# Performance work log

Measured on AMD Instinct MI355X. Metric: run time of the kernel, lower is better.

Reference implementation:

```python
import jax, jax.numpy as jnp
import numpy as np

NSAMPLE = 16
LEAKY = 0.1


def _leaky(x):
    return jnp.where(x >= 0, x, LEAKY * x)


def _sqdist(src, dst):
    # src [B,N,3], dst [B,M,3] -> [B,N,M]
    d = -2.0 * jnp.einsum('bnc,bmc->bnm', src, dst)
    d = d + jnp.sum(src * src, -1)[:, :, None]
    d = d + jnp.sum(dst * dst, -1)[:, None, :]
    return d


def _knn_idx(query, points, k):
    # query [B,N,3], points [B,M,3] -> [B,N,k] indices of k nearest points
    dist = _sqdist(query, points)
    _, idx = jax.lax.top_k(-dist, k)
    return idx


def _group(points, idx):
    # points [B,M,C], idx [B,N,K] -> [B,N,K,C]
    return jax.vmap(lambda p, i: p[i])(points, idx)


def _cross(xyz1, xyz2, p1, p2, pos_w, pos_b, mlp_params):
    # xyz1 [B,N1,3], xyz2 [B,N2,3], p1 [B,N1,C], p2 [B,N2,C]
    idx = _knn_idx(xyz1, xyz2, NSAMPLE)                       # [B,N1,K]
    neigh_xyz = _group(xyz2, idx)                             # [B,N1,K,3]
    direction = neigh_xyz - xyz1[:, :, None, :]               # [B,N1,K,3]
    g2 = _group(p2, idx)                                      # [B,N1,K,C]
    pos_feat = jnp.einsum('bnkc,oc->bnko', direction, pos_w) + pos_b
    new_pts = _leaky(g2 + p1[:, :, None, :] + pos_feat)       # [B,N1,K,C0]
    for w, b in mlp_params:
        new_pts = _leaky(jnp.einsum('bnkc,oc->bnko', new_pts, w) + b)
    return jnp.max(new_pts, axis=2)                           # [B,N1,Cl]


def setup_inputs() -> dict:
    key = jax.random.key(0)
    ks = jax.random.split(key, 14)
    B, N, D = 2, 8192, 64
    s = 0.1
    return {
        'pc1': jax.random.normal(ks[0], (B, N, 3), jnp.float32),
        'pc2': jax.random.normal(ks[1], (B, N, 3), jnp.float32),
        'feat1': jax.random.normal(ks[2], (B, N, D), jnp.float32),
        'feat2': jax.random.normal(ks[3], (B, N, D), jnp.float32),
        'pos_w': jax.random.normal(ks[4], (64, 3), jnp.float32) * s,
        'pos_b': jax.random.normal(ks[5], (64,), jnp.float32) * s,
        'mlp_w0': jax.random.normal(ks[6], (64, 64), jnp.float32) * s,
        'mlp_b0': jax.random.normal(ks[7], (64,), jnp.float32) * s,
        'mlp_w1': jax.random.normal(ks[8], (64, 64), jnp.float32) * s,
        'mlp_b1': jax.random.normal(ks[9], (64,), jnp.float32) * s,
        't1_w': jax.random.normal(ks[10], (128, 64), jnp.float32) * s,
        't1_b': jax.random.normal(ks[11], (128,), jnp.float32) * s,
        't2_w': jax.random.normal(ks[12], (128, 64), jnp.float32) * s,
        't2_b': jax.random.normal(ks[13], (128,), jnp.float32) * s,
    }


def reference(pc1, pc2, feat1, feat2, pos_w, pos_b, mlp_w0, mlp_b0,
              mlp_w1, mlp_b1, t1_w, t1_b, t2_w, t2_b):
    mlp = [(mlp_w0, mlp_b0), (mlp_w1, mlp_b1)]
    f1 = _cross(pc1, pc2, feat1, feat2, pos_w, pos_b, mlp)    # [B,N1,64]
    f1 = jnp.einsum('bnc,oc->bno', f1, t1_w) + t1_b           # [B,N1,128]
    f2 = _cross(pc2, pc1, feat2, feat1, pos_w, pos_b, mlp)
    f2 = jnp.einsum('bnc,oc->bno', f2, t2_w) + t2_b
    return f1, f2
```

## Files before the change

kernel.cpp:

```cpp
#include <hip/hip_runtime.h>

#define NPTS 8192
#define KNNK 16
#define NSLOT 17
#define LEAKY 0.1f

typedef short bf16x8 __attribute__((ext_vector_type(8)));
typedef float f32x4  __attribute__((ext_vector_type(4)));

#define KTH   1024
#define QPB   128
#define CHN   32
#define GQ    4
#define JP4   (NPTS / (CHN * 4))
#define BUFCAP 48

__global__ __launch_bounds__(KTH, 4) void knn_kernel(
    const float* __restrict__ pc1, const float* __restrict__ pc2,
    int* __restrict__ knn_out)
{
    __shared__ float sx[NPTS], sy[NPTS], sz[NPTS];
    __shared__ float sbuf[QPB][2 * BUFCAP];
    __shared__ float sthr[QPB];
    __shared__ int   scnt[QPB];

    const int t   = threadIdx.x;
    const int q0  = blockIdx.x * QPB;
    const int dir = q0 >> 14;
    const int b   = (q0 >> 13) & 1;

    const float* __restrict__ pq    = dir ? pc2 : pc1;
    const float* __restrict__ pcand = dir ? pc1 : pc2;

    const float* src = pcand + (size_t)b * NPTS * 3;
    for (int i = t; i < NPTS; i += KTH) {
        sx[i] = src[3 * i];
        sy[i] = src[3 * i + 1];
        sz[i] = src[3 * i + 2];
    }
    if (t < QPB) scnt[t] = 0;
    __syncthreads();

    const int ch = t & (CHN - 1);
    const int qg = t >> 5;
    const int n0 = q0 & (NPTS - 1);

    float q2x[GQ], q2y[GQ], q2z[GQ];
    #pragma unroll
    for (int g = 0; g < GQ; ++g) {
        const float* qp = pq + ((size_t)b * NPTS + n0 + qg * GQ + g) * 3;
        q2x[g] = -2.0f * qp[0];
        q2y[g] = -2.0f * qp[1];
        q2z[g] = -2.0f * qp[2];
    }

    float m1[GQ], m2[GQ];
    #pragma unroll
    for (int g = 0; g < GQ; ++g) { m1[g] = 3.0e38f; m2[g] = 3.0e38f; }

    #pragma unroll 2
    for (int j = 0; j < JP4; ++j) {
        const int i0 = j * 128 + 4 * ch;
        const f32x4 cx = *(const f32x4*)&sx[i0];
        const f32x4 cy = *(const f32x4*)&sy[i0];
        const f32x4 cz = *(const f32x4*)&sz[i0];
        f32x4 cn;
        #pragma unroll
        for (int c = 0; c < 4; ++c)
            cn[c] = fmaf(cx[c], cx[c], fmaf(cy[c], cy[c], cz[c] * cz[c]));
        #pragma unroll
        for (int g = 0; g < GQ; ++g) {
            #pragma unroll
            for (int c = 0; c < 4; ++c) {
                const float d = fmaf(q2x[g], cx[c],
                                fmaf(q2y[g], cy[c],
                                fmaf(q2z[g], cz[c], cn[c])));
                m2[g] = __builtin_amdgcn_fmed3f(d, m1[g], m2[g]);
                m1[g] = fminf(m1[g], d);
            }
        }
    }

    #pragma unroll
    for (int g = 0; g < GQ; ++g) {
        const int row = qg * GQ + g;
        sbuf[row][2 * ch]     = m1[g];
        sbuf[row][2 * ch + 1] = m2[g];
    }
    __builtin_amdgcn_wave_barrier();

    #pragma unroll
    for (int g = 0; g < GQ; ++g) {
        const int row = qg * GQ + g;
        const float v1 = m1[g], v2 = m2[g];
        int lt1 = 0, eq1 = 0, lt2 = 0, eq2 = 0;
        #pragma unroll
        for (int c = 0; c < 2 * CHN; c += 2) {
            const float2 vp = *(const float2*)&sbuf[row][c];
            lt1 += (vp.x < v1) ? 1 : 0;  eq1 += (vp.x == v1) ? 1 : 0;
            lt1 += (vp.y < v1) ? 1 : 0;  eq1 += (vp.y == v1) ? 1 : 0;
            lt2 += (vp.x < v2) ? 1 : 0;  eq2 += (vp.x == v2) ? 1 : 0;
            lt2 += (vp.y < v2) ? 1 : 0;  eq2 += (vp.y == v2) ? 1 : 0;
        }
        if (lt1 <= 16 && lt1 + eq1 > 16) sthr[row] = v1;
        if (lt2 <= 16 && lt2 + eq2 > 16) sthr[row] = v2;
    }
    __builtin_amdgcn_wave_barrier();

    float tq[GQ];
    #pragma unroll
    for (int g = 0; g < GQ; ++g) tq[g] = sthr[qg * GQ + g];

    #pragma unroll 2
    for (int j = 0; j < JP4; ++j) {
        const int i0 = j * 128 + 4 * ch;
        const f32x4 cx = *(const f32x4*)&sx[i0];
        const f32x4 cy = *(const f32x4*)&sy[i0];
        const f32x4 cz = *(const f32x4*)&sz[i0];
        f32x4 cn;
        #pragma unroll
        for (int c = 0; c < 4; ++c)
            cn[c] = fmaf(cx[c], cx[c], fmaf(cy[c], cy[c], cz[c] * cz[c]));
        #pragma unroll
        for (int g = 0; g < GQ; ++g) {
            #pragma unroll
            for (int c = 0; c < 4; ++c) {
                const float d = fmaf(q2x[g], cx[c],
                                fmaf(q2y[g], cy[c],
                                fmaf(q2z[g], cz[c], cn[c])));
                if (d <= tq[g]) {
                    const int q = qg * GQ + g;
                    const int pos = atomicAdd(&scnt[q], 1);
                    if (pos < BUFCAP) {
                        sbuf[q][pos] = d;
                        ((int*)&sbuf[q][BUFCAP])[pos] = i0 + c;
                    }
                }
            }
        }
    }
    __syncthreads();

    if (t < QPB) {
        const int nc = min(scnt[t], BUFCAP);

        float dist[NSLOT];
        int   ind[NSLOT];
        #pragma unroll
        for (int i = 0; i < NSLOT; ++i) { dist[i] = 3.0e38f; ind[i] = 0x7fffffff; }

        for (int s = 0; s < nc; ++s) {
            const float d  = sbuf[t][s];
            const int   id = ((int*)&sbuf[t][BUFCAP])[s];
            const bool better0 = (d < dist[0]) || (d == dist[0] && id < ind[0]);
            if (better0) {
                bool cprev = true;
                #pragma unroll
                for (int i = 0; i < NSLOT - 1; ++i) {
                    const bool ci = (d < dist[i + 1]) ||
                                    (d == dist[i + 1] && id < ind[i + 1]);
                    const float nv = ci ? dist[i + 1] : (cprev ? d  : dist[i]);
                    const int   ni = ci ? ind[i + 1]  : (cprev ? id : ind[i]);
                    dist[i] = nv; ind[i] = ni;
                    cprev = ci;
                }
                if (cprev) { dist[NSLOT - 1] = d; ind[NSLOT - 1] = id; }
            }
        }

        const float* qpp = pq + ((size_t)b * NPTS + n0 + t) * 3;
        const double dqx = (double)qpp[0], dqy = (double)qpp[1], dqz = (double)qpp[2];
        double dd[NSLOT];
        #pragma unroll
        for (int i = 0; i < NSLOT; ++i) {
            const int id = ind[i];
            const double dx = (double)sx[id] - dqx;
            const double dy = (double)sy[id] - dqy;
            const double dz = (double)sz[id] - dqz;
            dd[i] = dx * dx + dy * dy + dz * dz;
        }
        int worst = 0; double wd = dd[0];
        #pragma unroll
        for (int i = 1; i < NSLOT; ++i) { if (dd[i] > wd) { wd = dd[i]; worst = i; } }

        int* outp = knn_out + (size_t)(q0 + t) * KNNK;
        int slot = 0;
        #pragma unroll
        for (int i = 0; i < NSLOT; ++i) {
            if (i != worst) outp[slot++] = ind[i];
        }
    }
}

#define PTS 16
#define NG  4

__device__ __forceinline__ unsigned int packhl(float f) {
    const unsigned int u = __float_as_uint(f);
    const unsigned int h = u & 0xffff0000u;
    const float lf = f - __uint_as_float(h);
    return h | (__float_as_uint(lf) >> 16);
}

__device__ __forceinline__ void build_b(const float* __restrict__ wrow,
                                        bf16x8* hi, bf16x8* lo) {
    union { unsigned int u[4]; bf16x8 v; } H, L;
    #pragma unroll
    for (int r = 0; r < 4; ++r) {
        const float f0 = wrow[2 * r], f1 = wrow[2 * r + 1];
        const unsigned int h0 = __float_as_uint(f0) & 0xffff0000u;
        const unsigned int h1 = __float_as_uint(f1) & 0xffff0000u;
        const float l0 = f0 - __uint_as_float(h0);
        const float l1 = f1 - __uint_as_float(h1);
        H.u[r] = h1 | (h0 >> 16);
        L.u[r] = (__float_as_uint(l1) & 0xffff0000u) | (__float_as_uint(l0) >> 16);
    }
    *hi = H.v; *lo = L.v;
}

__device__ __forceinline__ void unpack_a(const unsigned int* __restrict__ Tu,
                                         bf16x8* hi, bf16x8* lo) {
    union { unsigned int u[4]; bf16x8 v; } H, L;
    #pragma unroll
    for (int r = 0; r < 4; ++r) {
        const unsigned int a = Tu[2 * r + 1], bb = Tu[2 * r];
        H.u[r] = __builtin_amdgcn_perm(a, bb, 0x07060302u);
        L.u[r] = __builtin_amdgcn_perm(a, bb, 0x05040100u);
    }
    *hi = H.v; *lo = L.v;
}

__device__ __forceinline__ f32x4 mfma3(f32x4 acc, bf16x8 ah, bf16x8 al,
                                       bf16x8 bh, bf16x8 bl) {
    acc = __builtin_amdgcn_mfma_f32_16x16x32_bf16(ah, bl, acc, 0, 0, 0);
    acc = __builtin_amdgcn_mfma_f32_16x16x32_bf16(al, bh, acc, 0, 0, 0);
    acc = __builtin_amdgcn_mfma_f32_16x16x32_bf16(ah, bh, acc, 0, 0, 0);
    return acc;
}

__global__ __launch_bounds__(256, 4) void feat_kernel(
    const float* __restrict__ pc1, const float* __restrict__ pc2,
    const float* __restrict__ feat1, const float* __restrict__ feat2,
    const float* __restrict__ pos_w, const float* __restrict__ pos_b,
    const float* __restrict__ w0, const float* __restrict__ b0,
    const float* __restrict__ w1, const float* __restrict__ b1,
    const float* __restrict__ t1w, const float* __restrict__ t1b,
    const float* __restrict__ t2w, const float* __restrict__ t2b,
    const int* __restrict__ knn, float* __restrict__ out)
{
    __shared__ unsigned int T0[4][16][68];
    __shared__ unsigned int T1[4][16][68];
    __shared__ float sm[PTS][64];

    const int t    = threadIdx.x;
    const int w    = t >> 6;
    const int lane = t & 63;
    const int m    = lane & 15;
    const int quad = lane >> 4;

    const int p0  = blockIdx.x * PTS;
    const int dir = p0 >> 14, bt = (p0 >> 13) & 1;
    const int n0  = p0 & (NPTS - 1);

    const float* __restrict__ pqd = dir ? pc2 : pc1;
    const float* __restrict__ pcd = dir ? pc1 : pc2;
    const float* __restrict__ fqd = dir ? feat2 : feat1;
    const float* __restrict__ fcd = dir ? feat1 : feat2;

    const int ocol = w * 16 + m;
    bf16x8 Bh[2][2], Bl[2][2];
    #pragma unroll
    for (int kt = 0; kt < 2; ++kt) {
        build_b(&w0[(size_t)ocol * 64 + kt * 32 + quad * 8], &Bh[0][kt], &Bl[0][kt]);
        build_b(&w1[(size_t)ocol * 64 + kt * 32 + quad * 8], &Bh[1][kt], &Bl[1][kt]);
    }
    const float bias1 = b0[ocol];
    const float bias2 = b1[ocol];

    const int cg0 = w * 16 + quad * 4;
    float pbc[4], pwx[4], pwy[4], pwz[4];
    #pragma unroll
    for (int i = 0; i < 4; ++i) {
        pbc[i] = pos_b[cg0 + i];
        pwx[i] = pos_w[(cg0 + i) * 3 + 0];
        pwy[i] = pos_w[(cg0 + i) * 3 + 1];
        pwz[i] = pos_w[(cg0 + i) * 3 + 2];
    }

    float  sdx[4], sdy[4], sdz[4];
    float4 sgf[4], sfq[4];

    auto loadg = [&](int gg) {
        #pragma unroll
        for (int pt = 0; pt < 4; ++pt) {
            const int pp = p0 + gg * 4 + pt;
            const int nn = n0 + gg * 4 + pt;
            const int id = knn[(size_t)pp * KNNK + m];
            const float* qp  = pqd + ((size_t)bt * NPTS + nn) * 3;
            const float* nbp = pcd + ((size_t)bt * NPTS + id) * 3;
            sdx[pt] = nbp[0] - qp[0];
            sdy[pt] = nbp[1] - qp[1];
            sdz[pt] = nbp[2] - qp[2];
            sgf[pt] = *(const float4*)&fcd[((size_t)bt * NPTS + id) * 64 + cg0];
            sfq[pt] = *(const float4*)&fqd[((size_t)bt * NPTS + nn) * 64 + cg0];
        }
    };

    auto storeg = [&]() {
        #pragma unroll
        for (int pt = 0; pt < 4; ++pt) {
            const float gfa[4] = {sgf[pt].x, sgf[pt].y, sgf[pt].z, sgf[pt].w};
            const float fqa[4] = {sfq[pt].x, sfq[pt].y, sfq[pt].z, sfq[pt].w};
            uint4 U;
            unsigned int* Up = (unsigned int*)&U;
            #pragma unroll
            for (int i = 0; i < 4; ++i) {
                float v = gfa[i] + fqa[i] + pbc[i];
                v = fmaf(sdx[pt], pwx[i], v);
                v = fmaf(sdy[pt], pwy[i], v);
                v = fmaf(sdz[pt], pwz[i], v);
                v = fmaxf(v, LEAKY * v);
                Up[i] = packhl(v);
            }
            *(uint4*)&T0[pt][m][cg0] = U;
        }
    };

    loadg(0);
    storeg();
    __syncthreads();

    #pragma unroll
    for (int g = 0; g < NG; ++g) {
        if (g + 1 < NG) loadg(g + 1);

        #pragma unroll
        for (int pt = 0; pt < 4; ++pt) {
            unsigned int Tu[8];
            bf16x8 Ah, Al;
            f32x4 acc = {0.f, 0.f, 0.f, 0.f};
            #pragma unroll
            for (int kt = 0; kt < 2; ++kt) {
                *(uint4*)&Tu[0] = *(const uint4*)&T0[pt][m][kt * 32 + quad * 8];
                *(uint4*)&Tu[4] = *(const uint4*)&T0[pt][m][kt * 32 + quad * 8 + 4];
                unpack_a(Tu, &Ah, &Al);
                acc = mfma3(acc, Ah, Al, Bh[0][kt], Bl[0][kt]);
            }
            #pragma unroll
            for (int r = 0; r < 4; ++r) {
                float v = acc[r] + bias1;
                v = fmaxf(v, LEAKY * v);
                T1[pt][quad * 4 + r][ocol] = packhl(v);
            }
        }
        __syncthreads();

        if (g + 1 < NG) storeg();

        #pragma unroll
        for (int pt = 0; pt < 4; ++pt) {
            unsigned int Tu[8];
            bf16x8 Ah, Al;
            f32x4 acc = {0.f, 0.f, 0.f, 0.f};
            #pragma unroll
            for (int kt = 0; kt < 2; ++kt) {
                *(uint4*)&Tu[0] = *(const uint4*)&T1[pt][m][kt * 32 + quad * 8];
                *(uint4*)&Tu[4] = *(const uint4*)&T1[pt][m][kt * 32 + quad * 8 + 4];
                unpack_a(Tu, &Ah, &Al);
                acc = mfma3(acc, Ah, Al, Bh[1][kt], Bl[1][kt]);
            }
            float mx = -3.0e38f;
            #pragma unroll
            for (int r = 0; r < 4; ++r) {
                float v = acc[r] + bias2;
                v = fmaxf(v, LEAKY * v);
                mx = fmaxf(mx, v);
            }
            mx = fmaxf(mx, __shfl_xor(mx, 16));
            mx = fmaxf(mx, __shfl_xor(mx, 32));
            if (quad == 0) sm[g * 4 + pt][ocol] = mx;
        }
        __syncthreads();
    }

    {
        const float* __restrict__ tw = dir ? t2w : t1w;
        const float* __restrict__ tb = dir ? t2b : t1b;
        const int o  = t & 127;
        const int pg = t >> 7;
        float acc[8];
        const float bz = tb[o];
        #pragma unroll
        for (int i = 0; i < 8; ++i) acc[i] = bz;
        #pragma unroll
        for (int cc = 0; cc < 64; cc += 4) {
            const float4 wq = *(const float4*)&tw[(size_t)o * 64 + cc];
            #pragma unroll
            for (int pr = 0; pr < 4; ++pr) {
                const int pa = (2 * pr + pg) * 2;
                const float4 a0 = *(const float4*)&sm[pa][cc];
                const float4 a1 = *(const float4*)&sm[pa + 1][cc];
                float x0 = acc[2 * pr], x1 = acc[2 * pr + 1];
                x0 = fmaf(a0.x, wq.x, x0); x0 = fmaf(a0.y, wq.y, x0);
                x0 = fmaf(a0.z, wq.z, x0); x0 = fmaf(a0.w, wq.w, x0);
                x1 = fmaf(a1.x, wq.x, x1); x1 = fmaf(a1.y, wq.y, x1);
                x1 = fmaf(a1.z, wq.z, x1); x1 = fmaf(a1.w, wq.w, x1);
                acc[2 * pr] = x0; acc[2 * pr + 1] = x1;
            }
        }
        float* op = out + (size_t)dir * (2 * NPTS * 128);
        #pragma unroll
        for (int pr = 0; pr < 4; ++pr) {
            const int pa = (2 * pr + pg) * 2;
            op[((size_t)bt * NPTS + n0 + pa) * 128 + o]     = acc[2 * pr];
            op[((size_t)bt * NPTS + n0 + pa + 1) * 128 + o] = acc[2 * pr + 1];
        }
    }
}

extern "C" void kernel_launch(void* const* d_in, const int* in_sizes, int n_in,
                              void* d_out, int out_size, void* d_ws, size_t ws_size,
                              hipStream_t stream)
{
    const float* pc1   = (const float*)d_in[0];
    const float* pc2   = (const float*)d_in[1];
    const float* feat1 = (const float*)d_in[2];
    const float* feat2 = (const float*)d_in[3];
    const float* pos_w = (const float*)d_in[4];
    const float* pos_b = (const float*)d_in[5];
    const float* w0    = (const float*)d_in[6];
    const float* b0    = (const float*)d_in[7];
    const float* w1    = (const float*)d_in[8];
    const float* b1    = (const float*)d_in[9];
    const float* t1w   = (const float*)d_in[10];
    const float* t1b   = (const float*)d_in[11];
    const float* t2w   = (const float*)d_in[12];
    const float* t2b   = (const float*)d_in[13];

    int*   knn = (int*)d_ws;
    float* out = (float*)d_out;

    hipLaunchKernelGGL(knn_kernel, dim3(32768 / QPB), dim3(KTH), 0, stream,
                       pc1, pc2, knn);
    hipLaunchKernelGGL(feat_kernel, dim3(32768 / PTS), dim3(256), 0, stream,
                       pc1, pc2, feat1, feat2, pos_w, pos_b,
                       w0, b0, w1, b1, t1w, t1b, t2w, t2b, knn, out);
}
```

Before: 272.9 us.

## Compute KNN distances with split-bf16 MFMA and threshold slack, rescoring survivors in fp32

The brute-force distance scan in the KNN kernel moves from scalar FMAs to MFMA 16x16x32 bf16 instructions. Coordinates and norms are split into hi/lo bf16 pairs so the product approximates fp32 accuracy. Candidates are staged in two halves of packed uint4 entries to cut LDS use, and the per-channel top-2 minima are reduced across the wave split. Because the approximate distances are inexact, the second pass uses the threshold plus a small DELTA and recomputes survivor distances in fp32 from global memory before the sort. This adds restaging of the candidates in each pass and a risk of overflowing BUFCAP when many points fall within the slack.

Measured after the change: 293.4 us. 1.08x slower.

```diff
diff --git a/kernel.cpp b/kernel.cpp
--- a/kernel.cpp
+++ b/kernel.cpp
@@ -8,21 +8,30 @@
 typedef short bf16x8 __attribute__((ext_vector_type(8)));
 typedef float f32x4  __attribute__((ext_vector_type(4)));
 
-#define KTH   1024
-#define QPB   128
-#define CHN   32
-#define GQ    4
-#define JP4   (NPTS / (CHN * 4))
-#define BUFCAP 48
+#define KTH    1024
+#define QPB    128
+#define HALF   4096
+#define CT_H   (HALF / 16)
+#define BUFCAP 64
+#define DELTA  0.0078125f
+
+
+__device__ __forceinline__ unsigned short bfh(float f) {
+    return (unsigned short)(__float_as_uint(f) >> 16);
+}
+__device__ __forceinline__ float bfhf(float f) {
+    return __uint_as_float(__float_as_uint(f) & 0xffff0000u);
+}
 
 __global__ __launch_bounds__(KTH, 4) void knn_kernel(
     const float* __restrict__ pc1, const float* __restrict__ pc2,
     int* __restrict__ knn_out)
 {
-    __shared__ float sx[NPTS], sy[NPTS], sz[NPTS];
+    __shared__ uint4 cbuf[HALF];
     __shared__ float sbuf[QPB][2 * BUFCAP];
     __shared__ float sthr[QPB];
     __shared__ int   scnt[QPB];
+    __shared__ uint4 zb;
 
     const int t   = threadIdx.x;
     const int q0  = blockIdx.x * QPB;
@@ -31,112 +40,187 @@
 
     const float* __restrict__ pq    = dir ? pc2 : pc1;
     const float* __restrict__ pcand = dir ? pc1 : pc2;
-
-    const float* src = pcand + (size_t)b * NPTS * 3;
-    for (int i = t; i < NPTS; i += KTH) {
-        sx[i] = src[3 * i];
-        sy[i] = src[3 * i + 1];
-        sz[i] = src[3 * i + 2];
-    }
+    const float* __restrict__ csrc  = pcand + (size_t)b * NPTS * 3;
+    const int n0 = q0 & (NPTS - 1);
+
+    const int lane = t & 63;
+    const int wave = t >> 6;
+    const int col  = lane & 15;
+    const int quad = lane >> 4;
+    const int qg   = wave & 3;
+    const int cs   = wave >> 2;
+
     if (t < QPB) scnt[t] = 0;
-    __syncthreads();
-
-    const int ch = t & (CHN - 1);
-    const int qg = t >> 5;
-    const int n0 = q0 & (NPTS - 1);
-
-    float q2x[GQ], q2y[GQ], q2z[GQ];
-    #pragma unroll
-    for (int g = 0; g < GQ; ++g) {
-        const float* qp = pq + ((size_t)b * NPTS + n0 + qg * GQ + g) * 3;
-        q2x[g] = -2.0f * qp[0];
-        q2y[g] = -2.0f * qp[1];
-        q2z[g] = -2.0f * qp[2];
-    }
-
-    float m1[GQ], m2[GQ];
-    #pragma unroll
-    for (int g = 0; g < GQ; ++g) { m1[g] = 3.0e38f; m2[g] = 3.0e38f; }
-
-    #pragma unroll 2
-    for (int j = 0; j < JP4; ++j) {
-        const int i0 = j * 128 + 4 * ch;
-        const f32x4 cx = *(const f32x4*)&sx[i0];
-        const f32x4 cy = *(const f32x4*)&sy[i0];
-        const f32x4 cz = *(const f32x4*)&sz[i0];
-        f32x4 cn;
-        #pragma unroll
-        for (int c = 0; c < 4; ++c)
-            cn[c] = fmaf(cx[c], cx[c], fmaf(cy[c], cy[c], cz[c] * cz[c]));
-        #pragma unroll
-        for (int g = 0; g < GQ; ++g) {
-            #pragma unroll
-            for (int c = 0; c < 4; ++c) {
-                const float d = fmaf(q2x[g], cx[c],
-                                fmaf(q2y[g], cy[c],
-                                fmaf(q2z[g], cz[c], cn[c])));
-                m2[g] = __builtin_amdgcn_fmed3f(d, m1[g], m2[g]);
-                m1[g] = fminf(m1[g], d);
-            }
-        }
-    }
-
-    #pragma unroll
-    for (int g = 0; g < GQ; ++g) {
-        const int row = qg * GQ + g;
-        sbuf[row][2 * ch]     = m1[g];
-        sbuf[row][2 * ch + 1] = m2[g];
-    }
-    __builtin_amdgcn_wave_barrier();
-
-    #pragma unroll
-    for (int g = 0; g < GQ; ++g) {
-        const int row = qg * GQ + g;
-        const float v1 = m1[g], v2 = m2[g];
+    if (t == 0)  { zb.x = 0; zb.y = 0; zb.z = 0; zb.w = 0; }
+
+    bf16x8 A1[2], A2[2];
+    #pragma unroll
+    for (int j = 0; j < 2; ++j) {
+        union { unsigned short u[8]; bf16x8 v; } a1u, a2u;
+        #pragma unroll
+        for (int e = 0; e < 8; ++e) { a1u.u[e] = 0; a2u.u[e] = 0; }
+        if (quad == 0) {
+            const int aq = n0 + (2 * qg + j) * 16 + col;
+            const float* qp = pq + ((size_t)b * NPTS + aq) * 3;
+            const float fx = -2.0f * qp[0];
+            const float fy = -2.0f * qp[1];
+            const float fz = -2.0f * qp[2];
+            const unsigned short hx = bfh(fx), hy = bfh(fy), hz = bfh(fz);
+            const unsigned short lx = bfh(fx - bfhf(fx));
+            const unsigned short ly = bfh(fy - bfhf(fy));
+            const unsigned short lz = bfh(fz - bfhf(fz));
+            a1u.u[0] = hx; a1u.u[1] = hy; a1u.u[2] = hz; a1u.u[3] = 0x3F80;
+            a1u.u[4] = lx; a1u.u[5] = ly; a1u.u[6] = lz; a1u.u[7] = 0x3F80;
+            a2u.u[0] = lx; a2u.u[1] = ly; a2u.u[2] = lz; a2u.u[3] = 0;
+            a2u.u[4] = hx; a2u.u[5] = hy; a2u.u[6] = hz; a2u.u[7] = 0;
+        }
+        A1[j] = a1u.v; A2[j] = a2u.v;
+    }
+
+    auto stage = [&](int h) {
+        for (int i = t; i < HALF; i += KTH) {
+            const int gi = h * HALF + i;
+            const float cx = csrc[3 * gi];
+            const float cy = csrc[3 * gi + 1];
+            const float cz = csrc[3 * gi + 2];
+            const float cn = fmaf(cx, cx, fmaf(cy, cy, cz * cz));
+            const unsigned int hx = bfh(cx), hy = bfh(cy), hz = bfh(cz), hn = bfh(cn);
+            const unsigned int lx = bfh(cx - bfhf(cx));
+            const unsigned int ly = bfh(cy - bfhf(cy));
+            const unsigned int lz = bfh(cz - bfhf(cz));
+            const unsigned int ln = bfh(cn - bfhf(cn));
+            uint4 e;
+            e.x = hx | (hy << 16);
+            e.y = hz | (hn << 16);
+            e.z = lx | (ly << 16);
+            e.w = lz | (ln << 16);
+            cbuf[i] = e;
+        }
+    };
+
+    const int  bstep = (quad == 0) ? 4 * 16 * (int)sizeof(uint4) : 0;
+    const char* bbase0 = (quad == 0)
+        ? (const char*)&cbuf[cs * 16 + col] : (const char*)&zb;
+
+    float m1t[2][4], m2t[2][4];
+    #pragma unroll
+    for (int j = 0; j < 2; ++j)
+        #pragma unroll
+        for (int r = 0; r < 4; ++r) { m1t[j][r] = 3.0e38f; m2t[j][r] = 3.0e38f; }
+
+    #pragma unroll
+    for (int h = 0; h < 2; ++h) {
+        __syncthreads();
+        stage(h);
+        __syncthreads();
+        const char* bp = bbase0;
+        #pragma unroll 2
+        for (int ct = cs; ct < CT_H; ct += 4) {
+            const bf16x8 B = *(const bf16x8*)bp; bp += bstep;
+            #pragma unroll
+            for (int j = 0; j < 2; ++j) {
+                f32x4 d = {0.f, 0.f, 0.f, 0.f};
+                d = __builtin_amdgcn_mfma_f32_16x16x32_bf16(A1[j], B, d, 0, 0, 0);
+                d = __builtin_amdgcn_mfma_f32_16x16x32_bf16(A2[j], B, d, 0, 0, 0);
+                #pragma unroll
+                for (int r = 0; r < 4; ++r) {
+                    m2t[j][r] = __builtin_amdgcn_fmed3f(d[r], m1t[j][r], m2t[j][r]);
+                    m1t[j][r] = fminf(m1t[j][r], d[r]);
+                }
+            }
+        }
+    }
+    __syncthreads();
+
+    #pragma unroll
+    for (int j = 0; j < 2; ++j)
+        #pragma unroll
+        for (int r = 0; r < 4; ++r) {
+            const int row = (2 * qg + j) * 16 + quad * 4 + r;
+            const int ch  = cs * 16 + col;
+            sbuf[row][2 * ch]     = m1t[j][r];
+            sbuf[row][2 * ch + 1] = m2t[j][r];
+        }
+    __syncthreads();
+
+    float* mt = (float*)cbuf;
+    for (int tau = t; tau < QPB * 32; tau += KTH) {
+        const int q = tau >> 5, j = tau & 31;
+        const float a1 = sbuf[q][2 * j],        a2 = sbuf[q][2 * j + 1];
+        const float b1 = sbuf[q][2 * (j + 32)], b2 = sbuf[q][2 * (j + 32) + 1];
+        mt[q * 64 + 2 * j]     = fminf(a1, b1);
+        mt[q * 64 + 2 * j + 1] = fminf(fmaxf(a1, b1), fminf(a2, b2));
+    }
+    __syncthreads();
+    for (int tau = t; tau < QPB * 32; tau += KTH) {
+        const int q = tau >> 5, j = tau & 31;
+        const float v1 = mt[q * 64 + 2 * j], v2 = mt[q * 64 + 2 * j + 1];
         int lt1 = 0, eq1 = 0, lt2 = 0, eq2 = 0;
         #pragma unroll
-        for (int c = 0; c < 2 * CHN; c += 2) {
-            const float2 vp = *(const float2*)&sbuf[row][c];
+        for (int c = 0; c < 64; c += 2) {
+            const float2 vp = *(const float2*)&mt[q * 64 + c];
             lt1 += (vp.x < v1) ? 1 : 0;  eq1 += (vp.x == v1) ? 1 : 0;
             lt1 += (vp.y < v1) ? 1 : 0;  eq1 += (vp.y == v1) ? 1 : 0;
             lt2 += (vp.x < v2) ? 1 : 0;  eq2 += (vp.x == v2) ? 1 : 0;
             lt2 += (vp.y < v2) ? 1 : 0;  eq2 += (vp.y == v2) ? 1 : 0;
         }
-        if (lt1 <= 16 && lt1 + eq1 > 16) sthr[row] = v1;
-        if (lt2 <= 16 && lt2 + eq2 > 16) sthr[row] = v2;
-    }
-    __builtin_amdgcn_wave_barrier();
-
-    float tq[GQ];
-    #pragma unroll
-    for (int g = 0; g < GQ; ++g) tq[g] = sthr[qg * GQ + g];
-
-    #pragma unroll 2
-    for (int j = 0; j < JP4; ++j) {
-        const int i0 = j * 128 + 4 * ch;
-        const f32x4 cx = *(const f32x4*)&sx[i0];
-        const f32x4 cy = *(const f32x4*)&sy[i0];
-        const f32x4 cz = *(const f32x4*)&sz[i0];
-        f32x4 cn;
-        #pragma unroll
-        for (int c = 0; c < 4; ++c)
-            cn[c] = fmaf(cx[c], cx[c], fmaf(cy[c], cy[c], cz[c] * cz[c]));
-        #pragma unroll
-        for (int g = 0; g < GQ; ++g) {
-            #pragma unroll
-            for (int c = 0; c < 4; ++c) {
-                const float d = fmaf(q2x[g], cx[c],
-                                fmaf(q2y[g], cy[c],
-                                fmaf(q2z[g], cz[c], cn[c])));
-                if (d <= tq[g]) {
-                    const int q = qg * GQ + g;
-                    const int pos = atomicAdd(&scnt[q], 1);
-                    if (pos < BUFCAP) {
-                        sbuf[q][pos] = d;
-                        ((int*)&sbuf[q][BUFCAP])[pos] = i0 + c;
+        if (lt1 <= 16 && lt1 + eq1 > 16) sthr[q] = v1;
+        if (lt2 <= 16 && lt2 + eq2 > 16) sthr[q] = v2;
+    }
+    __syncthreads();
+
+    float tq[2][4];
+    #pragma unroll
+    for (int j = 0; j < 2; ++j)
+        #pragma unroll
+        for (int r = 0; r < 4; ++r)
+            tq[j][r] = sthr[(2 * qg + j) * 16 + quad * 4 + r] + DELTA;
+
+    #pragma unroll
+    for (int h = 0; h < 2; ++h) {
+        __syncthreads();
+        stage(h);
+        __syncthreads();
+        const char* bp = bbase0;
+        #pragma unroll 2
+        for (int ct = cs; ct < CT_H; ct += 4) {
+            const bf16x8 B = *(const bf16x8*)bp; bp += bstep;
+            #pragma unroll
+            for (int j = 0; j < 2; ++j) {
+                f32x4 d = {0.f, 0.f, 0.f, 0.f};
+                d = __builtin_amdgcn_mfma_f32_16x16x32_bf16(A1[j], B, d, 0, 0, 0);
+                d = __builtin_amdgcn_mfma_f32_16x16x32_bf16(A2[j], B, d, 0, 0, 0);
+                const float g = fmaxf(fmaxf(tq[j][0] - d[0], tq[j][1] - d[1]),
+                                      fmaxf(tq[j][2] - d[2], tq[j][3] - d[3]));
+                if (g >= 0.f) {
+                    #pragma unroll
+                    for (int r = 0; r < 4; ++r) {
+                        if (d[r] <= tq[j][r]) {
+                            const int q = (2 * qg + j) * 16 + quad * 4 + r;
+                            const int pos = atomicAdd(&scnt[q], 1);
+                            if (pos < BUFCAP)
+                                ((int*)&sbuf[q][BUFCAP])[pos] =
+                                    h * HALF + ct * 16 + col;
+                        }
                     }
                 }
             }
+        }
+    }
+    __syncthreads();
+
+    {
+        const int rq = t >> 3;
+        const int nc = min(scnt[rq], BUFCAP);
+        const float* qp = pq + ((size_t)b * NPTS + n0 + rq) * 3;
+        const float q2x = -2.0f * qp[0];
+        const float q2y = -2.0f * qp[1];
+        const float q2z = -2.0f * qp[2];
+        for (int s = t & 7; s < nc; s += 8) {
+            const int id = ((int*)&sbuf[rq][BUFCAP])[s];
+            const float cx = csrc[3 * id], cy = csrc[3 * id + 1], cz = csrc[3 * id + 2];
+            const float cn = fmaf(cx, cx, fmaf(cy, cy, cz * cz));
+            sbuf[rq][s] = fmaf(q2x, cx, fmaf(q2y, cy, fmaf(q2z, cz, cn)));
         }
     }
     __syncthreads();
@@ -174,9 +258,10 @@
         #pragma unroll
         for (int i = 0; i < NSLOT; ++i) {
             const int id = ind[i];
-            const double dx = (double)sx[id] - dqx;
-            const double dy = (double)sy[id] - dqy;
-            const double dz = (double)sz[id] - dqz;
+            const float* cp = csrc + 3 * (size_t)id;
+            const double dx = (double)cp[0] - dqx;
+            const double dy = (double)cp[1] - dqy;
+            const double dz = (double)cp[2] - dqz;
             dd[i] = dx * dx + dy * dy + dz * dz;
         }
         int worst = 0; double wd = dd[0];
```
